# Kernel optimization log

Measured on AMD Instinct MI355X. Metric: run time of the kernel, lower is better.

The kernel has to match this reference:

```python
import jax, jax.numpy as jnp
import numpy as np

B, L, D_IN, D_MODEL, H = 8, 1024, 256, 512, 8
D_HEAD = D_MODEL // H


def setup_inputs() -> dict:
    key = jax.random.key(0)
    ks = jax.random.split(key, 12)
    queries = jax.random.normal(ks[0], (B, L, D_IN), dtype=jnp.float32)
    keys_ = jax.random.normal(ks[1], (B, L, D_IN), dtype=jnp.float32)
    values = jax.random.normal(ks[2], (B, L, D_IN), dtype=jnp.float32)
    attention_mask = jnp.ones((B, L), dtype=jnp.int32)
    # binary symmetric-ish adjacency (sparse molecular graph style)
    adjacency_matrix = (jax.random.uniform(ks[3], (B, L, L)) < 0.05).astype(jnp.float32)
    distance_matrix = jax.random.uniform(ks[4], (B, L, L), dtype=jnp.float32) * 10.0
    s = 1.0 / np.sqrt(D_IN)
    W_q = jax.random.normal(ks[5], (D_MODEL, D_IN), dtype=jnp.float32) * s
    W_k = jax.random.normal(ks[6], (D_MODEL, D_IN), dtype=jnp.float32) * s
    W_v = jax.random.normal(ks[7], (D_MODEL, D_IN), dtype=jnp.float32) * s
    W_o = jax.random.normal(ks[8], (D_MODEL, D_MODEL), dtype=jnp.float32) / np.sqrt(D_MODEL)
    lambda_a = jax.random.normal(ks[9], (H,), dtype=jnp.float32) * 0.1
    lambda_d = jax.random.normal(ks[10], (H,), dtype=jnp.float32) * 0.1
    return {"queries": queries, "keys": keys_, "values": values,
            "attention_mask": attention_mask, "adjacency_matrix": adjacency_matrix,
            "distance_matrix": distance_matrix, "W_q": W_q, "W_k": W_k,
            "W_v": W_v, "W_o": W_o, "lambda_a": lambda_a, "lambda_d": lambda_d}


def _split_heads(x):
    # (b, l, d_model) -> (b, h, l, d_head)
    b, l, _ = x.shape
    return x.reshape(b, l, H, D_HEAD).transpose(0, 2, 1, 3)


def reference(queries, keys, values, attention_mask, adjacency_matrix,
              distance_matrix, W_q, W_k, W_v, W_o, lambda_a, lambda_d):
    Q = _split_heads(queries @ W_q.T)   # (b,h,l,d)
    K = _split_heads(keys @ W_k.T)
    V = _split_heads(values @ W_v.T)
    scores = jnp.einsum("bhqd,bhkd->bhqk", Q, K) / jnp.sqrt(jnp.asarray(D_HEAD, Q.dtype))
    # MSRSA: per-head learned scalars inject graph structure into the scores
    scores = (scores
              + lambda_a[None, :, None, None] * adjacency_matrix[:, None, :, :]
              + lambda_d[None, :, None, None] * distance_matrix[:, None, :, :])
    mask = attention_mask[:, None, None, :] > 0  # (b,1,1,l) key mask
    scores = jnp.where(mask, scores, jnp.asarray(-1e9, scores.dtype))
    attn_weight = jax.nn.softmax(scores, axis=-1)  # (b,h,l,l)
    out = jnp.einsum("bhqk,bhkd->bhqd", attn_weight, V)
    out = out.transpose(0, 2, 1, 3).reshape(queries.shape[0], queries.shape[1], D_MODEL)
    return out @ W_o.T
```

## Files before the change

### kernel.cpp

```cpp
#include <hip/hip_runtime.h>
#include <hip/hip_fp16.h>

#define BB 8
#define LL 1024
#define DIN 256
#define DM 512
#define HH 8
#define DH 64

typedef __attribute__((ext_vector_type(8))) short bf16x8;
typedef __attribute__((ext_vector_type(4))) float f32x4;

__device__ __forceinline__ unsigned short f2bf(float f) {
  union { float f; unsigned u; } c; c.f = f;
  unsigned u = c.u;
  return (unsigned short)((u + 0x7fffu + ((u >> 16) & 1u)) >> 16);
}

#if defined(__has_builtin)
#if __has_builtin(__builtin_amdgcn_cvt_pk_bf16_f32)
#define HAS_PK_BF16 1
#endif
#endif

#ifdef HAS_PK_BF16
typedef __bf16 bf2 __attribute__((ext_vector_type(2)));
__device__ __forceinline__ unsigned pk2(float lo, float hi) {
  union { bf2 v; unsigned u; } c;
  c.v = __builtin_amdgcn_cvt_pk_bf16_f32(lo, hi);
  return c.u;
}
#else
__device__ __forceinline__ unsigned pk2(float lo, float hi) {
  return ((unsigned)f2bf(hi) << 16) | f2bf(lo);
}
#endif

__device__ __forceinline__ unsigned pkh(float a, float d) {
  return (unsigned)__half_as_ushort(__float2half_rn(a)) |
         ((unsigned)__half_as_ushort(__float2half_rn(d)) << 16);
}

__device__ __forceinline__ void async_copy16(void* lds, const void* g) {
  __builtin_amdgcn_global_load_lds(
      (const __attribute__((address_space(1))) unsigned*)g,
      (__attribute__((address_space(3))) unsigned*)lds, 16, 0, 0);
}

__global__ __launch_bounds__(256) void prep(
    const float* __restrict__ qin, const float* __restrict__ kin,
    const float* __restrict__ vin,
    const float* __restrict__ wq, const float* __restrict__ wk,
    const float* __restrict__ wv, const float* __restrict__ wo,
    const int* __restrict__ msk,
    const float* __restrict__ adj, const float* __restrict__ dis,
    unsigned short* __restrict__ xq, unsigned short* __restrict__ xk,
    unsigned short* __restrict__ xv,
    unsigned short* __restrict__ wqb, unsigned short* __restrict__ wkb,
    unsigned short* __restrict__ wvb, unsigned short* __restrict__ wob,
    float* __restrict__ mad, unsigned* __restrict__ bp)
{
  int t = blockIdx.x * 256 + threadIdx.x;
  const int XS = 524288, WS = 32768;
  if (t < 3 * XS) {
    int seg = t >> 19, off = t & (XS - 1);
    const float* s = (seg == 0) ? qin : (seg == 1) ? kin : vin;
    unsigned short* d = (seg == 0) ? xq : (seg == 1) ? xk : xv;
    float4 f = ((const float4*)s)[off];
    uint2 o = { pk2(f.x, f.y), pk2(f.z, f.w) };
    ((uint2*)d)[off] = o;
    return;
  }
  t -= 3 * XS;
  if (t < 3 * WS) {
    int seg = t >> 15, off = t & (WS - 1);
    const float* s = (seg == 0) ? wq : (seg == 1) ? wk : wv;
    unsigned short* d = (seg == 0) ? wqb : (seg == 1) ? wkb : wvb;
    float4 f = ((const float4*)s)[off];
    uint2 o = { pk2(f.x, f.y), pk2(f.z, f.w) };
    ((uint2*)d)[off] = o;
    return;
  }
  t -= 3 * WS;
  if (t < 65536) {
    float4 f = ((const float4*)wo)[t];
    uint2 o = { pk2(f.x, f.y), pk2(f.z, f.w) };
    ((uint2*)wob)[t] = o;
    return;
  }
  t -= 65536;
  if (t < 2048) {
    int4 m = ((const int4*)msk)[t];
    float4 f = { m.x ? 0.0f : -30000.0f, m.y ? 0.0f : -30000.0f,
                 m.z ? 0.0f : -30000.0f, m.w ? 0.0f : -30000.0f };
    ((float4*)mad)[t] = f;
    return;
  }
  t -= 2048;
  float4 a4 = ((const float4*)adj)[t];
  float4 d4 = ((const float4*)dis)[t];
  uint4 o = { pkh(a4.x, d4.x), pkh(a4.y, d4.y), pkh(a4.z, d4.z), pkh(a4.w, d4.w) };
  ((uint4*)bp)[t] = o;
}

__global__ __launch_bounds__(256) void qkv_proj(
    const unsigned short* __restrict__ xq, const unsigned short* __restrict__ xk,
    const unsigned short* __restrict__ xv,
    const unsigned short* __restrict__ wqb, const unsigned short* __restrict__ wkb,
    const unsigned short* __restrict__ wvb,
    unsigned short* __restrict__ qb, unsigned short* __restrict__ kb,
    unsigned short* __restrict__ vt)
{
  const int t = blockIdx.z;
  const unsigned short* __restrict__ X = (t == 0) ? xq : (t == 1) ? xk : xv;
  const unsigned short* __restrict__ W = (t == 0) ? wqb : (t == 1) ? wkb : wvb;
  const int m0 = blockIdx.y * 128;
  const int h  = blockIdx.x;
  __shared__ __align__(16) char arena[24576];
  const int tid = threadIdx.x;
  const int wid = tid >> 6;
  const int lane = tid & 63;
  const int lo = lane & 15;
  const int quad = lane >> 4;

  f32x4 acc[2][4];
#pragma unroll
  for (int mi = 0; mi < 2; ++mi)
#pragma unroll
    for (int ni = 0; ni < 4; ++ni) acc[mi][ni] = (f32x4)0.0f;

#pragma unroll
  for (int j = 0; j < 2; ++j) {
    int id = j * 256 + tid, r = id >> 2, c = id & 3;
    async_copy16(arena + j * 4096 + wid * 1024,
                 X + (size_t)(m0 + r) * DIN + ((c ^ (r & 3)) * 8));
  }
  {
    int id = tid, r = id >> 2, c = id & 3;
    async_copy16(arena + 16384 + wid * 1024,
                 W + (size_t)(h * 64 + r) * DIN + ((c ^ (r & 3)) * 8));
  }
  __syncthreads();

  for (int it = 0; it < 8; ++it) {
    const int p = it & 1;
    if (it < 7) {
      const int kk = (it + 1) * 32, q = 1 - p;
#pragma unroll
      for (int j = 0; j < 2; ++j) {
        int id = j * 256 + tid, r = id >> 2, c = id & 3;
        async_copy16(arena + q * 8192 + j * 4096 + wid * 1024,
                     X + (size_t)(m0 + r) * DIN + kk + ((c ^ (r & 3)) * 8));
      }
      {
        int id = tid, r = id >> 2, c = id & 3;
        async_copy16(arena + 16384 + q * 4096 + wid * 1024,
                     W + (size_t)(h * 64 + r) * DIN + kk + ((c ^ (r & 3)) * 8));
      }
    }
    const unsigned short* Ab = (const unsigned short*)(arena + p * 8192);
    const unsigned short* Bb = (const unsigned short*)(arena + 16384 + p * 4096);
    bf16x8 a[2], bfr[4];
#pragma unroll
    for (int mi = 0; mi < 2; ++mi) {
      int R = wid * 32 + mi * 16 + lo;
      a[mi] = *(const bf16x8*)&Ab[R * 32 + ((quad ^ (R & 3)) * 8)];
    }
#pragma unroll
    for (int ni = 0; ni < 4; ++ni) {
      int N = ni * 16 + lo;
      bfr[ni] = *(const bf16x8*)&Bb[N * 32 + ((quad ^ (N & 3)) * 8)];
    }
#pragma unroll
    for (int mi = 0; mi < 2; ++mi)
#pragma unroll
      for (int ni = 0; ni < 4; ++ni)
        acc[mi][ni] = __builtin_amdgcn_mfma_f32_16x16x32_bf16(
            a[mi], bfr[ni], acc[mi][ni], 0, 0, 0);
    __syncthreads();
  }

  const int b = m0 >> 10;
  const int lbase0 = (m0 & 1023) + wid * 32;
  if (t < 2) {
    unsigned short* dstp = (t == 0) ? qb : kb;
#pragma unroll
    for (int mi = 0; mi < 2; ++mi)
#pragma unroll
      for (int ni = 0; ni < 4; ++ni) {
        int d = ni * 16 + lo;
#pragma unroll
        for (int r = 0; r < 4; ++r) {
          int lb = lbase0 + mi * 16 + quad * 4 + r;
          dstp[((size_t)(b * HH + h) * LL + lb) * DH + d] = f2bf(acc[mi][ni][r]);
        }
      }
  } else {
#pragma unroll
    for (int mi = 0; mi < 2; ++mi)
#pragma unroll
      for (int ni = 0; ni < 4; ++ni) {
        int d = ni * 16 + lo;
        int lb = lbase0 + mi * 16 + quad * 4;
        uint2 o = { pk2(acc[mi][ni][0], acc[mi][ni][1]),
                    pk2(acc[mi][ni][2], acc[mi][ni][3]) };
        *(uint2*)&vt[((size_t)(b * HH + h) * DH + d) * LL + lb] = o;
      }
  }
}

__global__ __launch_bounds__(256) void attn(
    const unsigned short* __restrict__ qb, const unsigned short* __restrict__ kb,
    const unsigned short* __restrict__ vt,
    const float* __restrict__ mad, const unsigned* __restrict__ bp,
    const float* __restrict__ la_, const float* __restrict__ ld_,
    unsigned short* __restrict__ ao)
{
  const int bi = blockIdx.x;
  const int b  = bi & 7;
  const int hg = (bi >> 3) & 3;
  const int q0 = (bi >> 5) * 32;
  const int tid = threadIdx.x;
  const int wid = tid >> 6;
  const int lane = tid & 63;
  const int lo = lane & 15;
  const int quad = lane >> 4;
  const int h  = hg * 2 + (wid & 1);
  const int kh = wid >> 1;
  const int bh = b * HH + h;

  __shared__ __align__(16) char arena[59392];
  unsigned short* pbufw = (unsigned short*)(arena + 49152) + wid * 1280;
  float*          mgbuf = (float*)arena;

  const float LOG2E = 1.44269504f;
  const float la2 = la_[h] * LOG2E, ld2 = ld_[h] * LOG2E;
  const float sc2 = 0.125f * LOG2E;

  const unsigned short* qp = qb + ((size_t)bh * LL + q0) * DH;
  bf16x8 qB[2][2];
#pragma unroll
  for (int nj = 0; nj < 2; ++nj)
#pragma unroll
    for (int ki = 0; ki < 2; ++ki)
      qB[nj][ki] = *(const bf16x8*)&qp[(nj * 16 + lo) * DH + ki * 32 + quad * 8];

  const unsigned short* kp = kb + (size_t)bh * LL * DH;
  const unsigned short* vp = vt + (size_t)bh * DH * LL;
  const unsigned* bpp = bp + ((size_t)b * LL + q0) * LL;
  const float* mp = mad + b * LL;

  f32x4 o[4][2];
  float rs[2] = {0.0f, 0.0f};
#pragma unroll
  for (int md = 0; md < 4; ++md)
#pragma unroll
    for (int nj = 0; nj < 2; ++nj) o[md][nj] = (f32x4)0.0f;

  const int kbeg = kh * (LL / 2);
  const int r8 = lane >> 3, p8 = lane & 7;

  {
    const unsigned short* kg = kp + (size_t)kbeg * DH;
#pragma unroll
    for (int j = 0; j < 4; ++j)
      async_copy16(arena + wid * 4096 + j * 1024,
                   kg + (j * 8 + r8) * 64 + ((p8 ^ r8) * 8));
    if ((wid & 1) == 0) {
      const int khs = wid >> 1;
      const unsigned* bg = bpp + khs * (LL / 2);
#pragma unroll
      for (int j = 0; j < 4; ++j)
        async_copy16(arena + 32768 + khs * 4096 + j * 1024,
                     bg + (size_t)(j * 8 + r8) * LL + ((p8 ^ r8) * 4));
    }
  }
  __syncthreads();

  for (int jt = 0; jt < 16; ++jt) {
    const int p = jt & 1;
    const int k0 = kbeg + jt * 32;

    if (jt < 15) {
      const int kn = k0 + 32, q = 1 - p;
      const unsigned short* kg = kp + (size_t)kn * DH;
#pragma unroll
      for (int j = 0; j < 4; ++j)
        async_copy16(arena + q * 16384 + wid * 4096 + j * 1024,
                     kg + (j * 8 + r8) * 64 + ((p8 ^ r8) * 8));
      if ((wid & 1) == 0) {
        const int khs = wid >> 1;
        const unsigned* bg = bpp + khs * (LL / 2) + (jt + 1) * 32;
#pragma unroll
        for (int j = 0; j < 4; ++j)
          async_copy16(arena + 32768 + q * 8192 + khs * 4096 + j * 1024,
                       bg + (size_t)(j * 8 + r8) * LL + ((p8 ^ r8) * 4));
      }
    }

    bf16x8 vA[4];
#pragma unroll
    for (int md = 0; md < 4; ++md)
      vA[md] = *(const bf16x8*)&vp[(md * 16 + lo) * LL + k0 + quad * 8];
    f32x4 msv[2];
#pragma unroll
    for (int mi = 0; mi < 2; ++mi)
      msv[mi] = *(const f32x4*)&mp[k0 + mi * 16 + quad * 4];

    const unsigned short* kbf = (const unsigned short*)(arena + p * 16384) + wid * 2048;
    const unsigned* bbf = (const unsigned*)(arena + 32768 + p * 8192) + kh * 1024;

    bf16x8 kA[2][2];
#pragma unroll
    for (int mi = 0; mi < 2; ++mi)
#pragma unroll
      for (int ki = 0; ki < 2; ++ki)
        kA[mi][ki] = *(const bf16x8*)&kbf[(mi * 16 + lo) * 64 +
                                          (((ki * 4 + quad) ^ (lo & 7)) * 8)];
    f32x4 s[2][2];
#pragma unroll
    for (int mi = 0; mi < 2; ++mi)
#pragma unroll
      for (int nj = 0; nj < 2; ++nj) s[mi][nj] = (f32x4)0.0f;
#pragma unroll
    for (int ki = 0; ki < 2; ++ki)
#pragma unroll
      for (int mi = 0; mi < 2; ++mi)
#pragma unroll
        for (int nj = 0; nj < 2; ++nj)
          s[mi][nj] = __builtin_amdgcn_mfma_f32_16x16x32_bf16(
              kA[mi][ki], qB[nj][ki], s[mi][nj], 0, 0, 0);

#pragma unroll
    for (int mi = 0; mi < 2; ++mi)
#pragma unroll
      for (int nj = 0; nj < 2; ++nj) {
        uint4 u = *(const uint4*)&bbf[(nj * 16 + lo) * 32 +
                                      (((mi * 4 + quad) ^ (lo & 7)) * 4)];
        float p4[4];
#pragma unroll
        for (int r = 0; r < 4; ++r) {
          union { unsigned v; __half2 hh; } c; c.v = u[r];
          float tt = fmaf(__high2float(c.hh), ld2, msv[mi][r]);
          tt = fmaf(__low2float(c.hh), la2, tt);
          p4[r] = __builtin_amdgcn_exp2f(fmaf(s[mi][nj][r], sc2, tt));
        }
        rs[nj] += (p4[0] + p4[1]) + (p4[2] + p4[3]);
        uint2 w = { pk2(p4[0], p4[1]), pk2(p4[2], p4[3]) };
        *(uint2*)&pbufw[(nj * 16 + lo) * 40 + mi * 16 + quad * 4] = w;
      }

    asm volatile("s_waitcnt lgkmcnt(0)" ::: "memory");

    bf16x8 pB[2];
#pragma unroll
    for (int nj = 0; nj < 2; ++nj)
      pB[nj] = *(const bf16x8*)&pbufw[(nj * 16 + lo) * 40 + quad * 8];

#pragma unroll
    for (int md = 0; md < 4; ++md)
#pragma unroll
      for (int nj = 0; nj < 2; ++nj)
        o[md][nj] = __builtin_amdgcn_mfma_f32_16x16x32_bf16(
            vA[md], pB[nj], o[md][nj], 0, 0, 0);

    __syncthreads();
  }

  const int hs = wid & 1;
  if (kh == 1) {
#pragma unroll
    for (int md = 0; md < 4; ++md)
#pragma unroll
      for (int nj = 0; nj < 2; ++nj)
#pragma unroll
        for (int r = 0; r < 4; ++r)
          mgbuf[hs * 2176 + ((md * 2 + nj) * 4 + r) * 64 + lane] = o[md][nj][r];
    mgbuf[hs * 2176 + 32 * 64 + lane] = rs[0];
    mgbuf[hs * 2176 + 33 * 64 + lane] = rs[1];
  }
  __syncthreads();
  if (kh == 0) {
#pragma unroll
    for (int md = 0; md < 4; ++md)
#pragma unroll
      for (int nj = 0; nj < 2; ++nj)
#pragma unroll
        for (int r = 0; r < 4; ++r)
          o[md][nj][r] += mgbuf[hs * 2176 + ((md * 2 + nj) * 4 + r) * 64 + lane];
    rs[0] += mgbuf[hs * 2176 + 32 * 64 + lane];
    rs[1] += mgbuf[hs * 2176 + 33 * 64 + lane];
    float inv[2];
#pragma unroll
    for (int nj = 0; nj < 2; ++nj) {
      rs[nj] += __shfl_xor(rs[nj], 16);
      rs[nj] += __shfl_xor(rs[nj], 32);
      inv[nj] = __builtin_amdgcn_rcpf(rs[nj]);
    }
#pragma unroll
    for (int md = 0; md < 4; ++md)
#pragma unroll
      for (int nj = 0; nj < 2; ++nj) {
        int l = q0 + nj * 16 + lo;
        uint2 st = { pk2(o[md][nj][0] * inv[nj], o[md][nj][1] * inv[nj]),
                     pk2(o[md][nj][2] * inv[nj], o[md][nj][3] * inv[nj]) };
        *(uint2*)&ao[((size_t)b * LL + l) * DM + h * DH + md * 16 + quad * 4] = st;
      }
  }
}

__global__ __launch_bounds__(256) void oproj(
    const unsigned short* __restrict__ ao, const unsigned short* __restrict__ wob,
    float* __restrict__ out)
{
  const int m0 = blockIdx.y * 128;
  const int n0 = blockIdx.x * 64;
  __shared__ __align__(16) char arena[24576];
  const int tid = threadIdx.x;
  const int wid = tid >> 6;
  const int lane = tid & 63;
  const int lo = lane & 15;
  const int quad = lane >> 4;

  f32x4 acc[2][4];
#pragma unroll
  for (int mi = 0; mi < 2; ++mi)
#pragma unroll
    for (int ni = 0; ni < 4; ++ni) acc[mi][ni] = (f32x4)0.0f;

#pragma unroll
  for (int j = 0; j < 2; ++j) {
    int id = j * 256 + tid, r = id >> 2, c = id & 3;
    async_copy16(arena + j * 4096 + wid * 1024,
                 ao + (size_t)(m0 + r) * DM + ((c ^ (r & 3)) * 8));
  }
  {
    int id = tid, r = id >> 2, c = id & 3;
    async_copy16(arena + 16384 + wid * 1024,
                 wob + (size_t)(n0 + r) * DM + ((c ^ (r & 3)) * 8));
  }
  __syncthreads();

  for (int it = 0; it < 16; ++it) {
    const int p = it & 1;
    if (it < 15) {
      const int kk = (it + 1) * 32, q = 1 - p;
#pragma unroll
      for (int j = 0; j < 2; ++j) {
        int id = j * 256 + tid, r = id >> 2, c = id & 3;
        async_copy16(arena + q * 8192 + j * 4096 + wid * 1024,
                     ao + (size_t)(m0 + r) * DM + kk + ((c ^ (r & 3)) * 8));
      }
      {
        int id = tid, r = id >> 2, c = id & 3;
        async_copy16(arena + 16384 + q * 4096 + wid * 1024,
                     wob + (size_t)(n0 + r) * DM + kk + ((c ^ (r & 3)) * 8));
      }
    }
    const unsigned short* Ab = (const unsigned short*)(arena + p * 8192);
    const unsigned short* Bb = (const unsigned short*)(arena + 16384 + p * 4096);
    bf16x8 a[2], bfr[4];
#pragma unroll
    for (int mi = 0; mi < 2; ++mi) {
      int R = wid * 32 + mi * 16 + lo;
      a[mi] = *(const bf16x8*)&Ab[R * 32 + ((quad ^ (R & 3)) * 8)];
    }
#pragma unroll
    for (int ni = 0; ni < 4; ++ni) {
      int N = ni * 16 + lo;
      bfr[ni] = *(const bf16x8*)&Bb[N * 32 + ((quad ^ (N & 3)) * 8)];
    }
#pragma unroll
    for (int mi = 0; mi < 2; ++mi)
#pragma unroll
      for (int ni = 0; ni < 4; ++ni)
        acc[mi][ni] = __builtin_amdgcn_mfma_f32_16x16x32_bf16(
            a[mi], bfr[ni], acc[mi][ni], 0, 0, 0);
    __syncthreads();
  }

#pragma unroll
  for (int mi = 0; mi < 2; ++mi)
#pragma unroll
    for (int ni = 0; ni < 4; ++ni)
#pragma unroll
      for (int r = 0; r < 4; ++r)
        out[(size_t)(m0 + wid * 32 + mi * 16 + quad * 4 + r) * DM +
            n0 + ni * 16 + lo] = acc[mi][ni][r];
}

extern "C" void kernel_launch(void* const* d_in, const int* in_sizes, int n_in,
                              void* d_out, int out_size, void* d_ws, size_t ws_size,
                              hipStream_t stream) {
  const float* qin = (const float*)d_in[0];
  const float* kin = (const float*)d_in[1];
  const float* vin = (const float*)d_in[2];
  const int*   msk = (const int*)d_in[3];
  const float* adj = (const float*)d_in[4];
  const float* dis = (const float*)d_in[5];
  const float* wq  = (const float*)d_in[6];
  const float* wk  = (const float*)d_in[7];
  const float* wv  = (const float*)d_in[8];
  const float* wo  = (const float*)d_in[9];
  const float* la  = (const float*)d_in[10];
  const float* ld  = (const float*)d_in[11];
  float* out = (float*)d_out;

  const size_t tensb = (size_t)BB * HH * LL * DH;
  const size_t xsz   = (size_t)BB * LL * DIN;
  unsigned short* qb  = (unsigned short*)d_ws;
  unsigned short* kb  = qb + tensb;
  unsigned short* vt  = kb + tensb;
  unsigned short* ao  = vt + tensb;
  unsigned short* xq  = ao;
  unsigned short* xk  = ao + xsz;
  unsigned short* xv  = ao + tensb;
  unsigned short* wqb = xv + xsz;
  unsigned short* wkb = wqb + (size_t)DM * DIN;
  unsigned short* wvb = wkb + (size_t)DM * DIN;
  unsigned short* wob = wvb + (size_t)DM * DIN;
  float*          mdd = (float*)(wob + (size_t)DM * DM);
  unsigned*       bpk = (unsigned*)(mdd + (size_t)BB * LL);

  prep<<<dim3(14984), 256, 0, stream>>>(qin, kin, vin, wq, wk, wv, wo, msk,
                                        adj, dis,
                                        xq, xk, xv, wqb, wkb, wvb, wob, mdd, bpk);
  qkv_proj<<<dim3(8, 64, 3), 256, 0, stream>>>(xq, xk, xv, wqb, wkb, wvb, qb, kb, vt);
  attn<<<dim3(1024), 256, 0, stream>>>(qb, kb, vt, mdd, bpk, la, ld, ao);
  oproj<<<dim3(8, 64), 256, 0, stream>>>(ao, wob, out);
}
```

Baseline: 233.9 us.

## Drop LDS double-buffering in attention, load K and bias directly from global

```diff
diff --git a/kernel.cpp b/kernel.cpp
--- a/kernel.cpp
+++ b/kernel.cpp
@@ -21,6 +21,9 @@
 #if __has_builtin(__builtin_amdgcn_cvt_pk_bf16_f32)
 #define HAS_PK_BF16 1
 #endif
+#if __has_builtin(__builtin_amdgcn_fdot2)
+#define HAS_FDOT2 1
+#endif
 #endif
 
 #ifdef HAS_PK_BF16
@@ -35,6 +38,8 @@
   return ((unsigned)f2bf(hi) << 16) | f2bf(lo);
 }
 #endif
+
+typedef _Float16 h2f __attribute__((ext_vector_type(2)));
 
 __device__ __forceinline__ unsigned pkh(float a, float d) {
   return (unsigned)__half_as_ushort(__float2half_rn(a)) |
@@ -209,7 +214,7 @@
   }
 }
 
-__global__ __launch_bounds__(256) void attn(
+__global__ __launch_bounds__(256, 4) void attn(
     const unsigned short* __restrict__ qb, const unsigned short* __restrict__ kb,
     const unsigned short* __restrict__ vt,
     const float* __restrict__ mad, const unsigned* __restrict__ bp,
@@ -229,13 +234,18 @@
   const int kh = wid >> 1;
   const int bh = b * HH + h;
 
-  __shared__ __align__(16) char arena[59392];
-  unsigned short* pbufw = (unsigned short*)(arena + 49152) + wid * 1280;
+  __shared__ __align__(16) char arena[17408];
+  unsigned short* pbufw = (unsigned short*)arena + wid * 1280;
   float*          mgbuf = (float*)arena;
 
   const float LOG2E = 1.44269504f;
   const float la2 = la_[h] * LOG2E, ld2 = ld_[h] * LOG2E;
   const float sc2 = 0.125f * LOG2E;
+#ifdef HAS_FDOT2
+  h2f lam2;
+  lam2.x = (_Float16)la2;
+  lam2.y = (_Float16)ld2;
+#endif
 
   const unsigned short* qp = qb + ((size_t)bh * LL + q0) * DH;
   bf16x8 qB[2][2];
@@ -258,46 +268,17 @@
     for (int nj = 0; nj < 2; ++nj) o[md][nj] = (f32x4)0.0f;
 
   const int kbeg = kh * (LL / 2);
-  const int r8 = lane >> 3, p8 = lane & 7;
-
-  {
-    const unsigned short* kg = kp + (size_t)kbeg * DH;
-#pragma unroll
-    for (int j = 0; j < 4; ++j)
-      async_copy16(arena + wid * 4096 + j * 1024,
-                   kg + (j * 8 + r8) * 64 + ((p8 ^ r8) * 8));
-    if ((wid & 1) == 0) {
-      const int khs = wid >> 1;
-      const unsigned* bg = bpp + khs * (LL / 2);
-#pragma unroll
-      for (int j = 0; j < 4; ++j)
-        async_copy16(arena + 32768 + khs * 4096 + j * 1024,
-                     bg + (size_t)(j * 8 + r8) * LL + ((p8 ^ r8) * 4));
-    }
-  }
-  __syncthreads();
 
   for (int jt = 0; jt < 16; ++jt) {
-    const int p = jt & 1;
     const int k0 = kbeg + jt * 32;
 
-    if (jt < 15) {
-      const int kn = k0 + 32, q = 1 - p;
-      const unsigned short* kg = kp + (size_t)kn * DH;
-#pragma unroll
-      for (int j = 0; j < 4; ++j)
-        async_copy16(arena + q * 16384 + wid * 4096 + j * 1024,
-                     kg + (j * 8 + r8) * 64 + ((p8 ^ r8) * 8));
-      if ((wid & 1) == 0) {
-        const int khs = wid >> 1;
-        const unsigned* bg = bpp + khs * (LL / 2) + (jt + 1) * 32;
-#pragma unroll
-        for (int j = 0; j < 4; ++j)
-          async_copy16(arena + 32768 + q * 8192 + khs * 4096 + j * 1024,
-                       bg + (size_t)(j * 8 + r8) * LL + ((p8 ^ r8) * 4));
-      }
-    }
-
+    bf16x8 kA[2][2];
+#pragma unroll
+    for (int mi = 0; mi < 2; ++mi)
+#pragma unroll
+      for (int ki = 0; ki < 2; ++ki)
+        kA[mi][ki] = *(const bf16x8*)&kp[(size_t)(k0 + mi * 16 + lo) * DH +
+                                         ki * 32 + quad * 8];
     bf16x8 vA[4];
 #pragma unroll
     for (int md = 0; md < 4; ++md)
@@ -307,16 +288,6 @@
     for (int mi = 0; mi < 2; ++mi)
       msv[mi] = *(const f32x4*)&mp[k0 + mi * 16 + quad * 4];
 
-    const unsigned short* kbf = (const unsigned short*)(arena + p * 16384) + wid * 2048;
-    const unsigned* bbf = (const unsigned*)(arena + 32768 + p * 8192) + kh * 1024;
-
-    bf16x8 kA[2][2];
-#pragma unroll
-    for (int mi = 0; mi < 2; ++mi)
-#pragma unroll
-      for (int ki = 0; ki < 2; ++ki)
-        kA[mi][ki] = *(const bf16x8*)&kbf[(mi * 16 + lo) * 64 +
-                                          (((ki * 4 + quad) ^ (lo & 7)) * 8)];
     f32x4 s[2][2];
 #pragma unroll
     for (int mi = 0; mi < 2; ++mi)
@@ -335,15 +306,21 @@
     for (int mi = 0; mi < 2; ++mi)
 #pragma unroll
       for (int nj = 0; nj < 2; ++nj) {
-        uint4 u = *(const uint4*)&bbf[(nj * 16 + lo) * 32 +
-                                      (((mi * 4 + quad) ^ (lo & 7)) * 4)];
+        uint4 u = *(const uint4*)&bpp[(size_t)(nj * 16 + lo) * LL +
+                                      k0 + mi * 16 + quad * 4];
         float p4[4];
 #pragma unroll
         for (int r = 0; r < 4; ++r) {
+          float t = fmaf(s[mi][nj][r], sc2, msv[mi][r]);
+#ifdef HAS_FDOT2
+          union { unsigned v; h2f hv; } c; c.v = u[r];
+          p4[r] = __builtin_amdgcn_exp2f(
+              __builtin_amdgcn_fdot2(c.hv, lam2, t, false));
+#else
           union { unsigned v; __half2 hh; } c; c.v = u[r];
-          float tt = fmaf(__high2float(c.hh), ld2, msv[mi][r]);
-          tt = fmaf(__low2float(c.hh), la2, tt);
-          p4[r] = __builtin_amdgcn_exp2f(fmaf(s[mi][nj][r], sc2, tt));
+          float tt = fmaf(__high2float(c.hh), ld2, t);
+          p4[r] = __builtin_amdgcn_exp2f(fmaf(__low2float(c.hh), la2, tt));
+#endif
         }
         rs[nj] += (p4[0] + p4[1]) + (p4[2] + p4[3]);
         uint2 w = { pk2(p4[0], p4[1]), pk2(p4[2], p4[3]) };
@@ -363,10 +340,9 @@
       for (int nj = 0; nj < 2; ++nj)
         o[md][nj] = __builtin_amdgcn_mfma_f32_16x16x32_bf16(
             vA[md], pB[nj], o[md][nj], 0, 0, 0);
-
-    __syncthreads();
-  }
-
+  }
+
+  __syncthreads();
   const int hs = wid & 1;
   if (kh == 1) {
 #pragma unroll
```

Result: slower. 270.8 us (+15.7%).

## Load packed bias directly to registers and fold lambdas via fdot2

Applied to the files above, without the earlier changes.

```diff
diff --git a/kernel.cpp b/kernel.cpp
--- a/kernel.cpp
+++ b/kernel.cpp
@@ -10,6 +10,7 @@
 
 typedef __attribute__((ext_vector_type(8))) short bf16x8;
 typedef __attribute__((ext_vector_type(4))) float f32x4;
+typedef _Float16 h2f __attribute__((ext_vector_type(2)));
 
 __device__ __forceinline__ unsigned short f2bf(float f) {
   union { float f; unsigned u; } c; c.f = f;
@@ -23,7 +24,7 @@
 #endif
 #endif
 
-#ifdef HAS_PK_BF16
+#if defined(HAS_PK_BF16)
 typedef __bf16 bf2 __attribute__((ext_vector_type(2)));
 __device__ __forceinline__ unsigned pk2(float lo, float hi) {
   union { bf2 v; unsigned u; } c;
@@ -35,6 +36,16 @@
   return ((unsigned)f2bf(hi) << 16) | f2bf(lo);
 }
 #endif
+
+__device__ __forceinline__ float biasdot(unsigned u, h2f lam, float t) {
+#if defined(__HIP_DEVICE_COMPILE__)
+  union { unsigned v; h2f hv; } c; c.v = u;
+  return __builtin_amdgcn_fdot2(c.hv, lam, t, false);
+#else
+  (void)u; (void)lam;
+  return t;
+#endif
+}
 
 __device__ __forceinline__ unsigned pkh(float a, float d) {
   return (unsigned)__half_as_ushort(__float2half_rn(a)) |
@@ -229,13 +240,16 @@
   const int kh = wid >> 1;
   const int bh = b * HH + h;
 
-  __shared__ __align__(16) char arena[59392];
-  unsigned short* pbufw = (unsigned short*)(arena + 49152) + wid * 1280;
+  __shared__ __align__(16) char arena[43008];
+  unsigned short* pbufw = (unsigned short*)(arena + 32768) + wid * 1280;
   float*          mgbuf = (float*)arena;
 
   const float LOG2E = 1.44269504f;
   const float la2 = la_[h] * LOG2E, ld2 = ld_[h] * LOG2E;
   const float sc2 = 0.125f * LOG2E;
+  h2f lam2;
+  lam2.x = (_Float16)la2;
+  lam2.y = (_Float16)ld2;
 
   const unsigned short* qp = qb + ((size_t)bh * LL + q0) * DH;
   bf16x8 qB[2][2];
@@ -266,14 +280,6 @@
     for (int j = 0; j < 4; ++j)
       async_copy16(arena + wid * 4096 + j * 1024,
                    kg + (j * 8 + r8) * 64 + ((p8 ^ r8) * 8));
-    if ((wid & 1) == 0) {
-      const int khs = wid >> 1;
-      const unsigned* bg = bpp + khs * (LL / 2);
-#pragma unroll
-      for (int j = 0; j < 4; ++j)
-        async_copy16(arena + 32768 + khs * 4096 + j * 1024,
-                     bg + (size_t)(j * 8 + r8) * LL + ((p8 ^ r8) * 4));
-    }
   }
   __syncthreads();
 
@@ -288,14 +294,6 @@
       for (int j = 0; j < 4; ++j)
         async_copy16(arena + q * 16384 + wid * 4096 + j * 1024,
                      kg + (j * 8 + r8) * 64 + ((p8 ^ r8) * 8));
-      if ((wid & 1) == 0) {
-        const int khs = wid >> 1;
-        const unsigned* bg = bpp + khs * (LL / 2) + (jt + 1) * 32;
-#pragma unroll
-        for (int j = 0; j < 4; ++j)
-          async_copy16(arena + 32768 + q * 8192 + khs * 4096 + j * 1024,
-                       bg + (size_t)(j * 8 + r8) * LL + ((p8 ^ r8) * 4));
-      }
     }
 
     bf16x8 vA[4];
@@ -306,9 +304,15 @@
 #pragma unroll
     for (int mi = 0; mi < 2; ++mi)
       msv[mi] = *(const f32x4*)&mp[k0 + mi * 16 + quad * 4];
+    uint4 ub[2][2];
+#pragma unroll
+    for (int mi = 0; mi < 2; ++mi)
+#pragma unroll
+      for (int nj = 0; nj < 2; ++nj)
+        ub[mi][nj] = *(const uint4*)&bpp[(size_t)(nj * 16 + lo) * LL +
+                                         k0 + mi * 16 + quad * 4];
 
     const unsigned short* kbf = (const unsigned short*)(arena + p * 16384) + wid * 2048;
-    const unsigned* bbf = (const unsigned*)(arena + 32768 + p * 8192) + kh * 1024;
 
     bf16x8 kA[2][2];
 #pragma unroll
@@ -335,15 +339,11 @@
     for (int mi = 0; mi < 2; ++mi)
 #pragma unroll
       for (int nj = 0; nj < 2; ++nj) {
-        uint4 u = *(const uint4*)&bbf[(nj * 16 + lo) * 32 +
-                                      (((mi * 4 + quad) ^ (lo & 7)) * 4)];
         float p4[4];
 #pragma unroll
         for (int r = 0; r < 4; ++r) {
-          union { unsigned v; __half2 hh; } c; c.v = u[r];
-          float tt = fmaf(__high2float(c.hh), ld2, msv[mi][r]);
-          tt = fmaf(__low2float(c.hh), la2, tt);
-          p4[r] = __builtin_amdgcn_exp2f(fmaf(s[mi][nj][r], sc2, tt));
+          float tb = fmaf(s[mi][nj][r], sc2, msv[mi][r]);
+          p4[r] = __builtin_amdgcn_exp2f(biasdot(ub[mi][nj][r], lam2, tb));
         }
         rs[nj] += (p4[0] + p4[1]) + (p4[2] + p4[3]);
         uint2 w = { pk2(p4[0], p4[1]), pk2(p4[2], p4[3]) };
```

Result: slower. 253.1 us (+8.2%).

## Keep softmax probabilities in registers by permuting V k-order; fuse bias via fdot2

Applied to the files above, without the earlier changes.

```diff
diff --git a/kernel.cpp b/kernel.cpp
--- a/kernel.cpp
+++ b/kernel.cpp
@@ -10,6 +10,7 @@
 
 typedef __attribute__((ext_vector_type(8))) short bf16x8;
 typedef __attribute__((ext_vector_type(4))) float f32x4;
+typedef _Float16 h2f __attribute__((ext_vector_type(2)));
 
 __device__ __forceinline__ unsigned short f2bf(float f) {
   union { float f; unsigned u; } c; c.f = f;
@@ -23,7 +24,7 @@
 #endif
 #endif
 
-#ifdef HAS_PK_BF16
+#if defined(HAS_PK_BF16)
 typedef __bf16 bf2 __attribute__((ext_vector_type(2)));
 __device__ __forceinline__ unsigned pk2(float lo, float hi) {
   union { bf2 v; unsigned u; } c;
@@ -35,6 +36,16 @@
   return ((unsigned)f2bf(hi) << 16) | f2bf(lo);
 }
 #endif
+
+__device__ __forceinline__ float biasdot(unsigned u, h2f lam, float t) {
+#if defined(__HIP_DEVICE_COMPILE__)
+  union { unsigned v; h2f hv; } c; c.v = u;
+  return __builtin_amdgcn_fdot2(c.hv, lam, t, false);
+#else
+  (void)u; (void)lam;
+  return t;
+#endif
+}
 
 __device__ __forceinline__ unsigned pkh(float a, float d) {
   return (unsigned)__half_as_ushort(__float2half_rn(a)) |
@@ -229,13 +240,15 @@
   const int kh = wid >> 1;
   const int bh = b * HH + h;
 
-  __shared__ __align__(16) char arena[59392];
-  unsigned short* pbufw = (unsigned short*)(arena + 49152) + wid * 1280;
-  float*          mgbuf = (float*)arena;
+  __shared__ __align__(16) char arena[49152];
+  float* mgbuf = (float*)arena;
 
   const float LOG2E = 1.44269504f;
   const float la2 = la_[h] * LOG2E, ld2 = ld_[h] * LOG2E;
   const float sc2 = 0.125f * LOG2E;
+  h2f lam2;
+  lam2.x = (_Float16)la2;
+  lam2.y = (_Float16)ld2;
 
   const unsigned short* qp = qb + ((size_t)bh * LL + q0) * DH;
   bf16x8 qB[2][2];
@@ -300,16 +313,20 @@
 
     bf16x8 vA[4];
 #pragma unroll
-    for (int md = 0; md < 4; ++md)
-      vA[md] = *(const bf16x8*)&vp[(md * 16 + lo) * LL + k0 + quad * 8];
+    for (int md = 0; md < 4; ++md) {
+      const unsigned short* vr = &vp[(md * 16 + lo) * LL + k0 + quad * 4];
+      uint2 v0 = *(const uint2*)vr;
+      uint2 v1 = *(const uint2*)(vr + 16);
+      union { unsigned u[4]; bf16x8 v; } cc;
+      cc.u[0] = v0.x; cc.u[1] = v0.y; cc.u[2] = v1.x; cc.u[3] = v1.y;
+      vA[md] = cc.v;
+    }
     f32x4 msv[2];
 #pragma unroll
     for (int mi = 0; mi < 2; ++mi)
       msv[mi] = *(const f32x4*)&mp[k0 + mi * 16 + quad * 4];
 
     const unsigned short* kbf = (const unsigned short*)(arena + p * 16384) + wid * 2048;
-    const unsigned* bbf = (const unsigned*)(arena + 32768 + p * 8192) + kh * 1024;
-
     bf16x8 kA[2][2];
 #pragma unroll
     for (int mi = 0; mi < 2; ++mi)
@@ -331,6 +348,8 @@
           s[mi][nj] = __builtin_amdgcn_mfma_f32_16x16x32_bf16(
               kA[mi][ki], qB[nj][ki], s[mi][nj], 0, 0, 0);
 
+    const unsigned* bbf = (const unsigned*)(arena + 32768 + p * 8192) + kh * 1024;
+    unsigned pw[2][4];
 #pragma unroll
     for (int mi = 0; mi < 2; ++mi)
 #pragma unroll
@@ -340,22 +359,21 @@
         float p4[4];
 #pragma unroll
         for (int r = 0; r < 4; ++r) {
-          union { unsigned v; __half2 hh; } c; c.v = u[r];
-          float tt = fmaf(__high2float(c.hh), ld2, msv[mi][r]);
-          tt = fmaf(__low2float(c.hh), la2, tt);
-          p4[r] = __builtin_amdgcn_exp2f(fmaf(s[mi][nj][r], sc2, tt));
+          float tb = fmaf(s[mi][nj][r], sc2, msv[mi][r]);
+          p4[r] = __builtin_amdgcn_exp2f(biasdot(u[r], lam2, tb));
         }
         rs[nj] += (p4[0] + p4[1]) + (p4[2] + p4[3]);
-        uint2 w = { pk2(p4[0], p4[1]), pk2(p4[2], p4[3]) };
-        *(uint2*)&pbufw[(nj * 16 + lo) * 40 + mi * 16 + quad * 4] = w;
-      }
-
-    asm volatile("s_waitcnt lgkmcnt(0)" ::: "memory");
-
+        pw[nj][mi * 2]     = pk2(p4[0], p4[1]);
+        pw[nj][mi * 2 + 1] = pk2(p4[2], p4[3]);
+      }
     bf16x8 pB[2];
 #pragma unroll
-    for (int nj = 0; nj < 2; ++nj)
-      pB[nj] = *(const bf16x8*)&pbufw[(nj * 16 + lo) * 40 + quad * 8];
+    for (int nj = 0; nj < 2; ++nj) {
+      union { unsigned u[4]; bf16x8 v; } pc;
+      pc.u[0] = pw[nj][0]; pc.u[1] = pw[nj][1];
+      pc.u[2] = pw[nj][2]; pc.u[3] = pw[nj][3];
+      pB[nj] = pc.v;
+    }
 
 #pragma unroll
     for (int md = 0; md < 4; ++md)
```

Result: slower. 257.7 us (+10.1%).
